# Kernel tuning notes

Hardware: AMD Instinct MI355X
Metric: run time of the kernel (lower is better)

## Reference

```python
import jax, jax.numpy as jnp
import numpy as np

T, D, H, E, K = 8192, 1024, 1024, 8, 2
N = T * K  # total dispatched rows


def setup_inputs() -> dict:
    key = jax.random.key(0)
    ks = jax.random.split(key, 12)
    s = 1.0 / np.sqrt(D)
    inp = {
        # uniform, contiguous per-expert segments: 2048 rows each
        'offsets': jnp.arange(E + 1, dtype=jnp.int64 if jax.config.jax_enable_x64 else jnp.int32) * (N // E),
        'jagged': jax.random.normal(ks[0], (T, D), jnp.float32),
        'weight': jax.random.normal(ks[1], (E, D, H), jnp.float32) * s,
        'bias': jax.random.normal(ks[2], (E, H), jnp.float32) * 0.02,
        'index': jax.random.randint(ks[3], (N,), 0, T),
        'weight_p': jax.random.normal(ks[4], (E, D, H), jnp.float32) * s,
        'weight_out': jax.random.normal(ks[5], (E, H, D), jnp.float32) * (1.0 / np.sqrt(H)),
        'reverse_index': jax.random.randint(ks[6], (T, K), 0, N),
        'gates': jax.random.uniform(ks[7], (N,), jnp.float32),
        'gates_index': jax.random.randint(ks[8], (T, K), 0, N),
        'bias_p': jax.random.normal(ks[9], (E, H), jnp.float32) * 0.02,
        'bias_out': jax.random.normal(ks[10], (E, D), jnp.float32) * 0.02,
    }
    return inp


def reference(offsets, jagged, weight, bias, index, weight_p, weight_out,
              reverse_index, gates, gates_index, bias_p, bias_out):
    # dispatch: gather token features into expert-sorted order  [N, D]
    x = jagged[index]
    n = x.shape[0]
    n_experts = weight.shape[0]
    # contiguous segment id per dispatched row
    expert_id = jnp.searchsorted(offsets, jnp.arange(n), side='right') - 1
    y = jnp.zeros((n, weight_out.shape[-1]), dtype=x.dtype)
    for e in range(n_experts):  # fixed small expert count
        m = (expert_id == e)[:, None].astype(x.dtype)
        xe = x * m
        g = xe @ weight[e] + bias[e]        # gate proj  [N, H]
        u = xe @ weight_p[e] + bias_p[e]    # up proj    [N, H]
        h = jax.nn.silu(g) * u              # SwiGLU
        y = y + (h @ weight_out[e] + bias_out[e]) * m
    # combine: gather K expert outputs per token, weight by gates  [T, D]
    gathered = y[reverse_index]             # [T, K, D]
    gv = gates[gates_index]                 # [T, K]
    return jnp.einsum('tkd,tk->td', gathered, gv)
```

## Files before the change

kernel.cpp:

```cpp
#include <hip/hip_runtime.h>
#include <hip/hip_bf16.h>

#define T_TOK 8192
#define DDIM 1024
#define HDIM 1024
#define NEXP 8
#define KTOP 2
#define NROWS (T_TOK * KTOP)

typedef __attribute__((ext_vector_type(8))) short bf16x8;
typedef __attribute__((ext_vector_type(4))) float f32x4;

__device__ __forceinline__ unsigned short f2bf(float f) {
    unsigned u = __builtin_bit_cast(unsigned, f);
    u += 0x7fffu + ((u >> 16) & 1u);
    return (unsigned short)(u >> 16);
}
__device__ __forceinline__ float bf2f(unsigned short h) {
    return __builtin_bit_cast(float, (unsigned)h << 16);
}

__device__ __forceinline__ void gll16(const unsigned short* g, const unsigned short* l) {
    __builtin_amdgcn_global_load_lds(
        (const __attribute__((address_space(1))) unsigned int*)g,
        (__attribute__((address_space(3))) unsigned int*)l, 16, 0, 0);
}


__global__ __launch_bounds__(256) void cvt_bf16_k(const float* __restrict__ in,
                                                  unsigned short* __restrict__ out, int n4) {
    int i = blockIdx.x * 256 + threadIdx.x;
    if (i >= n4) return;
    float4 v = ((const float4*)in)[i];
    ushort4 o;
    o.x = f2bf(v.x); o.y = f2bf(v.y); o.z = f2bf(v.z); o.w = f2bf(v.w);
    ((ushort4*)out)[i] = o;
}

__global__ __launch_bounds__(256) void transpose_cast_k(const float* __restrict__ in,
                                                        unsigned short* __restrict__ out,
                                                        int R, int C) {
    __shared__ unsigned short tile[32][33];
    int m = blockIdx.z;
    const float* src = in + (size_t)m * R * C;
    unsigned short* dst = out + (size_t)m * R * C;
    int c0 = blockIdx.x * 32, r0 = blockIdx.y * 32;
    int tx = threadIdx.x & 31, ty = threadIdx.x >> 5;
#pragma unroll
    for (int i = 0; i < 32; i += 8)
        tile[ty + i][tx] = f2bf(src[(size_t)(r0 + ty + i) * C + c0 + tx]);
    __syncthreads();
#pragma unroll
    for (int i = 0; i < 32; i += 8)
        dst[(size_t)(c0 + ty + i) * R + r0 + tx] = tile[tx][ty + i];
}


constexpr int BM2 = 256, BN2 = 256, BK2 = 64;
constexpr int NT2 = DDIM / BK2;

template <int VARIANT>
__global__ __launch_bounds__(512) void gemm256_8q_k(
    const unsigned short* __restrict__ A, const int* __restrict__ rowidx, int lda,
    const unsigned short* __restrict__ Bt, const float* __restrict__ biasE,
    const unsigned short* __restrict__ Gin, unsigned short* __restrict__ Out,
    const int* __restrict__ offsets, int N, int K) {
    __shared__ __attribute__((aligned(16))) unsigned short lds[65536];

    const int nbn = N / BN2;
    int l = (blockIdx.x & 7) * 32 + (blockIdx.x >> 3);
    int brow = l / nbn, bcol = l % nbn;
    int row0 = brow * BM2, col0 = bcol * BN2;
    int e = 0;
    while (offsets[e + 1] <= row0) ++e;

    const unsigned short* Bte = Bt + (size_t)e * N * K;
    const float* bias = biasE + (size_t)e * N;

    int tid = threadIdx.x;
    int lane = tid & 63, wid = tid >> 6;
    int wm = wid >> 2, wn = wid & 3;
    int l15 = lane & 15, l4 = lane >> 4;

    int srow = lane >> 3;
    int c8 = ((lane & 7) ^ srow) * 8;
    const unsigned short* aS[2][2];
    const unsigned short* bS[2][2];
#pragma unroll
    for (int h = 0; h < 2; ++h)
#pragma unroll
        for (int q = 0; q < 2; ++q) {
            int r = (wid & 3) * 16 + q * 8 + srow + h * 64 + (wid >> 2) * 128;
            int ar = rowidx ? rowidx[row0 + r] : row0 + r;
            aS[h][q] = A + (size_t)ar * lda + c8;
            int cc = (wid & 1) * 16 + q * 8 + srow + h * 32 + (wid >> 1) * 64;
            bS[h][q] = Bte + (size_t)(col0 + cc) * K + c8;
        }
    unsigned wq = wid * 1024;

#define STG_A(BUF, H, T) { \
        gll16(aS[H][0] + (T) * BK2, lds + (BUF) * 16384 + (H) * 8192 + wq);       \
        gll16(aS[H][1] + (T) * BK2, lds + (BUF) * 16384 + (H) * 8192 + wq + 512); }
#define STG_B(BUF, H, T) { \
        gll16(bS[H][0] + (T) * BK2, lds + 32768 + (BUF) * 16384 + (H) * 8192 + wq);       \
        gll16(bS[H][1] + (T) * BK2, lds + 32768 + (BUF) * 16384 + (H) * 8192 + wq + 512); }

    const char* LB = (const char*)lds;
    int arow = (wm * 64 + l15) * 128;
    int brw = (wn * 32 + l15) * 128;
    int cx = l15 & 7;
    int ch0 = (l4 ^ cx) * 16;
    int ch1 = ((4 + l4) ^ cx) * 16;

    f32x4 acc[8][4] = {};
    bf16x8 fa[8], fb[4];

#define PHASE(BUF, QM, QN, LOADA, STG)                                        \
    {                                                                         \
        if (LOADA) {                                                          \
            const char* Ab_ = LB + (BUF) * 32768 + (QM) * 16384 + arow;       \
            _Pragma("unroll") for (int mi = 0; mi < 4; ++mi) {                \
                fa[mi]     = *(const bf16x8*)(Ab_ + mi * 2048 + ch0);         \
                fa[4 + mi] = *(const bf16x8*)(Ab_ + mi * 2048 + ch1);         \
            }                                                                 \
        }                                                                     \
        {                                                                     \
            const char* Bb_ = LB + 65536 + (BUF) * 32768 + (QN) * 16384 + brw;\
            fb[0] = *(const bf16x8*)(Bb_ + ch0);                              \
            fb[1] = *(const bf16x8*)(Bb_ + 2048 + ch0);                       \
            fb[2] = *(const bf16x8*)(Bb_ + ch1);                              \
            fb[3] = *(const bf16x8*)(Bb_ + 2048 + ch1);                       \
        }                                                                     \
        STG;                                                                  \
        __builtin_amdgcn_s_barrier();                                         \
        asm volatile("s_waitcnt lgkmcnt(0)" ::: "memory");                    \
        __builtin_amdgcn_sched_barrier(0);                                    \
        __builtin_amdgcn_s_setprio(1);                                        \
        _Pragma("unroll") for (int s = 0; s < 2; ++s)                         \
        _Pragma("unroll") for (int mi = 0; mi < 4; ++mi)                      \
        _Pragma("unroll") for (int n = 0; n < 2; ++n)                         \
            acc[(QM) * 4 + mi][(QN) * 2 + n] =                                \
                __builtin_amdgcn_mfma_f32_16x16x32_bf16(                      \
                    fa[s * 4 + mi], fb[s * 2 + n],                            \
                    acc[(QM) * 4 + mi][(QN) * 2 + n], 0, 0, 0);               \
        __builtin_amdgcn_s_setprio(0);                                        \
    }

#define TILE(BUF, OBUF, KT)                                                   \
    PHASE(BUF, 0, 0, true,  if ((KT) + 1 < NT2) STG_A(OBUF, 1, (KT) + 1))     \
    __builtin_amdgcn_s_barrier();                                             \
    PHASE(BUF, 0, 1, false, if ((KT) + 1 < NT2) STG_B(OBUF, 1, (KT) + 1))     \
    __builtin_amdgcn_s_barrier();                                             \
    PHASE(BUF, 1, 0, true,  if ((KT) + 2 < NT2) STG_A(BUF, 0, (KT) + 2))      \
    __builtin_amdgcn_s_barrier();                                             \
    PHASE(BUF, 1, 1, false, if ((KT) + 2 < NT2) STG_B(BUF, 0, (KT) + 2))      \
    if ((KT) <= NT2 - 3) {                                                    \
        asm volatile("s_waitcnt vmcnt(4)" ::: "memory");                      \
        __builtin_amdgcn_s_barrier();                                         \
    } else if ((KT) == NT2 - 2) {                                             \
        asm volatile("s_waitcnt vmcnt(0)" ::: "memory");                      \
        __builtin_amdgcn_s_barrier();                                         \
    }

    STG_A(0, 0, 0) STG_B(0, 0, 0) STG_A(0, 1, 0) STG_B(0, 1, 0)
    STG_A(1, 0, 1) STG_B(1, 0, 1)
    asm volatile("s_waitcnt vmcnt(4)" ::: "memory");
    __builtin_amdgcn_s_barrier();

#pragma unroll 1
    for (int t = 0; t < NT2; t += 2) {
        TILE(0, 1, t)
        TILE(1, 0, t + 1)
    }
#undef TILE
#undef PHASE
#undef STG_A
#undef STG_B

    float bv[4];
#pragma unroll
    for (int ni = 0; ni < 4; ++ni)
        bv[ni] = bias[col0 + wn * 64 + ni * 16 + l15];

#pragma unroll
    for (int mi = 0; mi < 8; ++mi) {
        int orow_b = row0 + wm * 128 + mi * 16 + l4 * 4;
#pragma unroll
        for (int ni = 0; ni < 4; ++ni) {
            int ocol = col0 + wn * 64 + ni * 16 + l15;
#pragma unroll
            for (int q = 0; q < 4; ++q) {
                size_t oidx = (size_t)(orow_b + q) * N + ocol;
                float v = acc[mi][ni][q] + bv[ni];
                if (VARIANT == 1) {
                    float g = bf2f(Gin[oidx]);
                    float s = g / (1.0f + __expf(-g));
                    v = s * v;
                }
                Out[oidx] = f2bf(v);
            }
        }
    }
}


__global__ __launch_bounds__(256) void combine_k(
    const unsigned short* __restrict__ Y, const int* __restrict__ rev,
    const float* __restrict__ gates, const int* __restrict__ gidx,
    float* __restrict__ out) {
    int t = blockIdx.x;
    int r0 = rev[2 * t], r1 = rev[2 * t + 1];
    float g0 = gates[gidx[2 * t]], g1 = gates[gidx[2 * t + 1]];
    const unsigned short* y0 = Y + (size_t)r0 * DDIM;
    const unsigned short* y1 = Y + (size_t)r1 * DDIM;
    int d = threadIdx.x * 4;
    ushort4 a = *(const ushort4*)(y0 + d);
    ushort4 b = *(const ushort4*)(y1 + d);
    float4 r;
    r.x = g0 * bf2f(a.x) + g1 * bf2f(b.x);
    r.y = g0 * bf2f(a.y) + g1 * bf2f(b.y);
    r.z = g0 * bf2f(a.z) + g1 * bf2f(b.z);
    r.w = g0 * bf2f(a.w) + g1 * bf2f(b.w);
    *(float4*)(out + (size_t)t * DDIM + d) = r;
}


extern "C" void kernel_launch(void* const* d_in, const int* in_sizes, int n_in,
                              void* d_out, int out_size, void* d_ws, size_t ws_size,
                              hipStream_t stream) {
    const int* offsets = (const int*)d_in[0];
    const float* jagged = (const float*)d_in[1];
    const float* weight = (const float*)d_in[2];
    const float* bias = (const float*)d_in[3];
    const int* index = (const int*)d_in[4];
    const float* weight_p = (const float*)d_in[5];
    const float* weight_out = (const float*)d_in[6];
    const int* rev = (const int*)d_in[7];
    const float* gates = (const float*)d_in[8];
    const int* gidx = (const int*)d_in[9];
    const float* bias_p = (const float*)d_in[10];
    const float* bias_out = (const float*)d_in[11];
    float* out = (float*)d_out;

    char* w = (char*)d_ws;
    unsigned short* jag_bf = (unsigned short*)w; w += (size_t)T_TOK * DDIM * 2;
    unsigned short* W1t    = (unsigned short*)w; w += (size_t)NEXP * DDIM * HDIM * 2;
    unsigned short* Wpt    = (unsigned short*)w; w += (size_t)NEXP * DDIM * HDIM * 2;
    unsigned short* Wot    = (unsigned short*)w; w += (size_t)NEXP * HDIM * DDIM * 2;
    unsigned short* g_ws   = (unsigned short*)w; w += (size_t)NROWS * HDIM * 2;
    unsigned short* h_ws   = (unsigned short*)w; w += (size_t)NROWS * HDIM * 2;
    unsigned short* y_ws   = g_ws;

    cvt_bf16_k<<<(T_TOK * DDIM / 4 + 255) / 256, 256, 0, stream>>>(jagged, jag_bf, T_TOK * DDIM / 4);
    transpose_cast_k<<<dim3(HDIM / 32, DDIM / 32, NEXP), 256, 0, stream>>>(weight, W1t, DDIM, HDIM);
    transpose_cast_k<<<dim3(HDIM / 32, DDIM / 32, NEXP), 256, 0, stream>>>(weight_p, Wpt, DDIM, HDIM);
    transpose_cast_k<<<dim3(DDIM / 32, HDIM / 32, NEXP), 256, 0, stream>>>(weight_out, Wot, HDIM, DDIM);

    const int grid = (NROWS / BM2) * (HDIM / BN2);

    gemm256_8q_k<0><<<grid, 512, 0, stream>>>(jag_bf, index, DDIM, W1t, bias, nullptr, g_ws,
                                              offsets, HDIM, DDIM);
    gemm256_8q_k<1><<<grid, 512, 0, stream>>>(jag_bf, index, DDIM, Wpt, bias_p, g_ws, h_ws,
                                              offsets, HDIM, DDIM);
    gemm256_8q_k<0><<<grid, 512, 0, stream>>>(h_ws, nullptr, HDIM, Wot, bias_out, nullptr, y_ws,
                                              offsets, DDIM, HDIM);
    combine_k<<<T_TOK, 256, 0, stream>>>(y_ws, rev, gates, gidx, out);
}
```

Baseline: 178.8 us.

## Restructure GEMM main loop into K-split phases with shared B fragments

Reorganizes the 256x256 GEMM inner loop so that each k-tile is processed in four phases split along the K half (ch0/ch1) and the M half, rather than quadrant by quadrant. B fragments for both N halves are loaded once per K half and reused across both M halves, which cuts redundant LDS reads. Each phase now issues 16 MFMAs instead of 16 with a different operand mix. The global-to-LDS staging order and vmcnt wait thresholds are reworked to fit, which changes the prefetch timing and raises the risk of LDS buffer hazards.

```diff
diff --git a/kernel.cpp b/kernel.cpp
--- a/kernel.cpp
+++ b/kernel.cpp
@@ -60,7 +60,7 @@
 constexpr int NT2 = DDIM / BK2;
 
 template <int VARIANT>
-__global__ __launch_bounds__(512) void gemm256_8q_k(
+__global__ __launch_bounds__(512) void gemm256_ks_k(
     const unsigned short* __restrict__ A, const int* __restrict__ rowidx, int lda,
     const unsigned short* __restrict__ Bt, const float* __restrict__ biasE,
     const unsigned short* __restrict__ Gin, unsigned short* __restrict__ Out,
@@ -113,69 +113,65 @@
     int ch1 = ((4 + l4) ^ cx) * 16;
 
     f32x4 acc[8][4] = {};
-    bf16x8 fa[8], fb[4];
-
-#define PHASE(BUF, QM, QN, LOADA, STG)                                        \
-    {                                                                         \
-        if (LOADA) {                                                          \
-            const char* Ab_ = LB + (BUF) * 32768 + (QM) * 16384 + arow;       \
-            _Pragma("unroll") for (int mi = 0; mi < 4; ++mi) {                \
-                fa[mi]     = *(const bf16x8*)(Ab_ + mi * 2048 + ch0);         \
-                fa[4 + mi] = *(const bf16x8*)(Ab_ + mi * 2048 + ch1);         \
-            }                                                                 \
-        }                                                                     \
-        {                                                                     \
-            const char* Bb_ = LB + 65536 + (BUF) * 32768 + (QN) * 16384 + brw;\
-            fb[0] = *(const bf16x8*)(Bb_ + ch0);                              \
-            fb[1] = *(const bf16x8*)(Bb_ + 2048 + ch0);                       \
-            fb[2] = *(const bf16x8*)(Bb_ + ch1);                              \
-            fb[3] = *(const bf16x8*)(Bb_ + 2048 + ch1);                       \
-        }                                                                     \
-        STG;                                                                  \
-        __builtin_amdgcn_s_barrier();                                         \
-        asm volatile("s_waitcnt lgkmcnt(0)" ::: "memory");                    \
-        __builtin_amdgcn_sched_barrier(0);                                    \
-        __builtin_amdgcn_s_setprio(1);                                        \
-        _Pragma("unroll") for (int s = 0; s < 2; ++s)                         \
-        _Pragma("unroll") for (int mi = 0; mi < 4; ++mi)                      \
-        _Pragma("unroll") for (int n = 0; n < 2; ++n)                         \
-            acc[(QM) * 4 + mi][(QN) * 2 + n] =                                \
-                __builtin_amdgcn_mfma_f32_16x16x32_bf16(                      \
-                    fa[s * 4 + mi], fb[s * 2 + n],                            \
-                    acc[(QM) * 4 + mi][(QN) * 2 + n], 0, 0, 0);               \
-        __builtin_amdgcn_s_setprio(0);                                        \
+    bf16x8 fa[4], fb0[4], fb1[4];
+
+#define RD_FA(BUF, QM, CH) {                                                  \
+        const char* Ab_ = LB + (BUF) * 32768 + (QM) * 16384 + arow;           \
+        fa[0] = *(const bf16x8*)(Ab_ + 0 * 2048 + (CH));                      \
+        fa[1] = *(const bf16x8*)(Ab_ + 1 * 2048 + (CH));                      \
+        fa[2] = *(const bf16x8*)(Ab_ + 2 * 2048 + (CH));                      \
+        fa[3] = *(const bf16x8*)(Ab_ + 3 * 2048 + (CH)); }
+#define RD_FB(BUF, FB, CH) {                                                  \
+        const char* Bb_ = LB + 65536 + (BUF) * 32768 + brw;                   \
+        FB[0] = *(const bf16x8*)(Bb_ + (CH));                                 \
+        FB[1] = *(const bf16x8*)(Bb_ + 2048 + (CH));                          \
+        FB[2] = *(const bf16x8*)(Bb_ + 16384 + (CH));                         \
+        FB[3] = *(const bf16x8*)(Bb_ + 16384 + 2048 + (CH)); }
+#define MFMA16(QM, FB)                                                        \
+    asm volatile("s_waitcnt lgkmcnt(0)" ::: "memory");                        \
+    __builtin_amdgcn_sched_barrier(0);                                        \
+    __builtin_amdgcn_s_setprio(1);                                            \
+    _Pragma("unroll") for (int mi = 0; mi < 4; ++mi)                          \
+    _Pragma("unroll") for (int ni = 0; ni < 4; ++ni)                          \
+        acc[(QM) * 4 + mi][ni] = __builtin_amdgcn_mfma_f32_16x16x32_bf16(     \
+            fa[mi], FB[ni], acc[(QM) * 4 + mi][ni], 0, 0, 0);                 \
+    __builtin_amdgcn_s_setprio(0);
+
+    STG_A(0, 0, 0) STG_A(0, 1, 0) STG_B(0, 0, 0) STG_B(0, 1, 0)
+    STG_A(1, 0, 1) STG_B(1, 0, 1) STG_B(1, 1, 1)
+    asm volatile("s_waitcnt vmcnt(6)" ::: "memory");
+    __builtin_amdgcn_s_barrier();
+
+#pragma unroll 1
+    for (int t = 0; t < NT2; ++t) {
+        int bc = t & 1, bo = bc ^ 1;
+        RD_FA(bc, 0, ch0)
+        RD_FB(bc, fb0, ch0)
+        if (t + 1 < NT2) STG_A(bo, 1, t + 1)
+        MFMA16(0, fb0)
+        __builtin_amdgcn_s_barrier();
+        RD_FA(bc, 0, ch1)
+        RD_FB(bc, fb1, ch1)
+        MFMA16(0, fb1)
+        __builtin_amdgcn_s_barrier();
+        RD_FA(bc, 1, ch0)
+        if (t + 2 < NT2) { STG_A(bc, 0, t + 2) STG_B(bc, 0, t + 2) }
+        MFMA16(1, fb0)
+        __builtin_amdgcn_s_barrier();
+        RD_FA(bc, 1, ch1)
+        if (t + 2 < NT2) STG_B(bc, 1, t + 2)
+        MFMA16(1, fb1)
+        if (t + 1 < NT2) {
+            if (t + 2 < NT2) { asm volatile("s_waitcnt vmcnt(6)" ::: "memory"); }
+            else             { asm volatile("s_waitcnt vmcnt(0)" ::: "memory"); }
+            __builtin_amdgcn_s_barrier();
+        }
     }
-
-#define TILE(BUF, OBUF, KT)                                                   \
-    PHASE(BUF, 0, 0, true,  if ((KT) + 1 < NT2) STG_A(OBUF, 1, (KT) + 1))     \
-    __builtin_amdgcn_s_barrier();                                             \
-    PHASE(BUF, 0, 1, false, if ((KT) + 1 < NT2) STG_B(OBUF, 1, (KT) + 1))     \
-    __builtin_amdgcn_s_barrier();                                             \
-    PHASE(BUF, 1, 0, true,  if ((KT) + 2 < NT2) STG_A(BUF, 0, (KT) + 2))      \
-    __builtin_amdgcn_s_barrier();                                             \
-    PHASE(BUF, 1, 1, false, if ((KT) + 2 < NT2) STG_B(BUF, 0, (KT) + 2))      \
-    if ((KT) <= NT2 - 3) {                                                    \
-        asm volatile("s_waitcnt vmcnt(4)" ::: "memory");                      \
-        __builtin_amdgcn_s_barrier();                                         \
-    } else if ((KT) == NT2 - 2) {                                             \
-        asm volatile("s_waitcnt vmcnt(0)" ::: "memory");                      \
-        __builtin_amdgcn_s_barrier();                                         \
-    }
-
-    STG_A(0, 0, 0) STG_B(0, 0, 0) STG_A(0, 1, 0) STG_B(0, 1, 0)
-    STG_A(1, 0, 1) STG_B(1, 0, 1)
-    asm volatile("s_waitcnt vmcnt(4)" ::: "memory");
-    __builtin_amdgcn_s_barrier();
-
-#pragma unroll 1
-    for (int t = 0; t < NT2; t += 2) {
-        TILE(0, 1, t)
-        TILE(1, 0, t + 1)
-    }
-#undef TILE
-#undef PHASE
+#undef MFMA16
+#undef RD_FB
+#undef RD_FA
+#undef STG_B
 #undef STG_A
-#undef STG_B
 
     float bv[4];
 #pragma unroll
@@ -258,11 +254,11 @@
 
     const int grid = (NROWS / BM2) * (HDIM / BN2);
 
-    gemm256_8q_k<0><<<grid, 512, 0, stream>>>(jag_bf, index, DDIM, W1t, bias, nullptr, g_ws,
+    gemm256_ks_k<0><<<grid, 512, 0, stream>>>(jag_bf, index, DDIM, W1t, bias, nullptr, g_ws,
                                               offsets, HDIM, DDIM);
-    gemm256_8q_k<1><<<grid, 512, 0, stream>>>(jag_bf, index, DDIM, Wpt, bias_p, g_ws, h_ws,
+    gemm256_ks_k<1><<<grid, 512, 0, stream>>>(jag_bf, index, DDIM, Wpt, bias_p, g_ws, h_ws,
                                               offsets, HDIM, DDIM);
-    gemm256_8q_k<0><<<grid, 512, 0, stream>>>(h_ws, nullptr, HDIM, Wot, bias_out, nullptr, y_ws,
+    gemm256_ks_k<0><<<grid, 512, 0, stream>>>(h_ws, nullptr, HDIM, Wot, bias_out, nullptr, y_ws,
                                               offsets, DDIM, HDIM);
     combine_k<<<T_TOK, 256, 0, stream>>>(y_ws, rev, gates, gidx, out);
 }
```

New measurement: 175.8 us. Within noise of the previous version (-1.7%).
